# Performance work log

Hardware: AMD Instinct MI355X
Metric: run time of the kernel (lower is better)

The kernel has to match this reference:

```python
import jax, jax.numpy as jnp
import numpy as np

DIM = 64
HEADS = 4
DIM_HEAD = 32
HIDDEN = HEADS * DIM_HEAD  # 128
EPS = 1e-5


def _layernorm_ch(x, g, b):
    # channel-dim LayerNorm (biased var), x: [b, c, n]
    mean = jnp.mean(x, axis=1, keepdims=True)
    var = jnp.var(x, axis=1, keepdims=True)  # unbiased=False
    return (x - mean) / jnp.sqrt(var + EPS) * g.reshape(1, -1, 1) + b.reshape(1, -1, 1)


def setup_inputs() -> dict:
    key = jax.random.key(0)
    ks = jax.random.split(key, 4)
    x = jax.random.normal(ks[0], (2, DIM, 32, 64, 64), dtype=jnp.float32)
    # 1x1x1 convs are channel matmuls; store weights as [out_ch, in_ch]
    w_qkv = jax.random.normal(ks[1], (HIDDEN * 3, DIM), dtype=jnp.float32) * (1.0 / np.sqrt(DIM))
    w_out = jax.random.normal(ks[2], (DIM, HIDDEN), dtype=jnp.float32) * (1.0 / np.sqrt(HIDDEN))
    b_out = jax.random.normal(ks[3], (DIM,), dtype=jnp.float32) * 0.02
    g1 = jnp.ones((DIM,), dtype=jnp.float32)
    b1 = jnp.zeros((DIM,), dtype=jnp.float32)
    g2 = jnp.ones((DIM,), dtype=jnp.float32)
    b2 = jnp.zeros((DIM,), dtype=jnp.float32)
    return {"x": x, "g1": g1, "b1": b1, "w_qkv": w_qkv, "w_out": w_out,
            "b_out": b_out, "g2": g2, "b2": b2}


def reference(x, g1, b1, w_qkv, w_out, b_out, g2, b2):
    b, c, *spatial = x.shape
    n = int(np.prod(spatial))
    scale = DIM_HEAD ** -0.5

    xf = x.reshape(b, c, n)
    xn = _layernorm_ch(xf, g1, b1)

    # 1x1x1 conv qkv projection (no bias)
    qkv = jnp.einsum('oc,bcn->bon', w_qkv, xn)  # [b, 3*hidden, n]
    qkv = qkv.reshape(b, 3, HEADS, DIM_HEAD, n)
    q, k, v = qkv[:, 0], qkv[:, 1], qkv[:, 2]   # each [b, h, d, n]

    q = jax.nn.softmax(q, axis=2) * scale       # softmax over dim_head
    k = jax.nn.softmax(k, axis=3)               # softmax over tokens

    ctx = jnp.einsum('bhdn,bhen->bhde', k, v)   # [b, h, d, e] small
    out = jnp.einsum('bhde,bhdn->bhen', ctx, q) # [b, h, e, n]
    out = out.reshape(b, HIDDEN, n)

    y = jnp.einsum('oc,bcn->bon', w_out, out) + b_out.reshape(1, -1, 1)
    y = _layernorm_ch(y, g2, b2)
    return y.reshape(b, c, *spatial)
```

## Files before the change

### kernel.cpp

```cpp
#include <hip/hip_runtime.h>

#define NCOL 131072
#define CH 64

typedef float floatx4 __attribute__((ext_vector_type(4)));
typedef __bf16 bf16x8 __attribute__((ext_vector_type(8)));
typedef unsigned int u32x4 __attribute__((ext_vector_type(4)));
typedef unsigned int u32x2 __attribute__((ext_vector_type(2)));

union FragU { u32x4 q; bf16x8 v; unsigned short us[8]; };

__device__ __forceinline__ unsigned short bfb(float f){
  union { __bf16 h; unsigned short s; } u; u.h = (__bf16)f; return u.s;
}
__device__ __forceinline__ float bf2f(unsigned short h){
  union { unsigned u; float f; } x{(unsigned)h << 16};
  return x.f;
}

__device__ __forceinline__ void ln_stage(const float* __restrict__ xp,
    const float* __restrict__ g, const float* __restrict__ bb,
    unsigned short* __restrict__ xn_s, int t)
{
  float xv[64]; float s = 0.f, ss = 0.f;
  #pragma unroll
  for (int c = 0; c < 64; c++){ float u = xp[(long)c*NCOL]; xv[c] = u; s += u; ss = fmaf(u,u,ss); }
  const float mean = s * (1.f/64.f);
  const float rstd = rsqrtf(ss * (1.f/64.f) - mean*mean + 1e-5f);
  #pragma unroll
  for (int c = 0; c < 64; c++) xv[c] = (xv[c]-mean)*rstd*g[c] + bb[c];
  #pragma unroll
  for (int j = 0; j < 8; j++){
    FragU u;
    #pragma unroll
    for (int e = 0; e < 8; e++) u.v[e] = (__bf16)xv[j*8+e];
    *(u32x4*)(xn_s + t*72 + j*8) = u.q;
  }
}

__global__ __launch_bounds__(256) void kW(
    const float* __restrict__ wqkv, unsigned short* __restrict__ wbf, float* __restrict__ Oz)
{
  const int i = blockIdx.x*256 + threadIdx.x;
  wbf[i] = bfb(wqkv[i]);
  if (i < 8448) Oz[i] = 0.f;
}

__global__ __launch_bounds__(256) void kA(
    const float* __restrict__ x, const float* __restrict__ g1, const float* __restrict__ b1,
    const unsigned short* __restrict__ wbf, float* __restrict__ pctx, float* __restrict__ Zg)
{
  __shared__ __align__(16) char smem[37888];
  unsigned short* xn_s = (unsigned short*)smem;
  unsigned short* ek_s = (unsigned short*)smem;
  unsigned short* v_s  = (unsigned short*)(smem + 16896);
  float* Zp            = (float*)(smem + 33792);

  const int t = threadIdx.x;
  const int bid = blockIdx.x;
  const int b = bid >> 9;
  const long col0 = (long)(bid & 511) * 256;
  const int w = t >> 6, lane = t & 63, qq = lane >> 4, l16 = lane & 15;

  ln_stage(x + (long)b*CH*NCOL + col0 + t, g1, b1, xn_s, t);
  FragU bx[4][2];
  #pragma unroll
  for (int nt = 0; nt < 4; nt++)
    #pragma unroll
    for (int ks = 0; ks < 2; ks++)
      bx[nt][ks].q = *(const u32x4*)(xn_s + ((4*w+nt)*16 + l16)*72 + ks*32 + qq*8);
  __syncthreads();

  floatx4 cc[4][2][2];
  #pragma unroll
  for (int h = 0; h < 4; h++)
    #pragma unroll
    for (int dt = 0; dt < 2; dt++)
      #pragma unroll
      for (int et = 0; et < 2; et++)
        cc[h][dt][et] = floatx4{0.f,0.f,0.f,0.f};

  #pragma unroll
  for (int h = 0; h < 4; h++){
    float zr[8];
    #pragma unroll
    for (int j = 0; j < 8; j++) zr[j] = 0.f;
    #pragma unroll
    for (int rt = 0; rt < 4; rt++){
      const int row0 = ((rt < 2) ? 128 : 256) + h*32 + (rt & 1)*16;
      const unsigned short* wr = wbf + (row0 + l16)*64 + qq*8;
      FragU a0, a1;
      a0.q = *(const u32x4*)wr;
      a1.q = *(const u32x4*)(wr + 32);
      unsigned short* dst = ((rt < 2) ? ek_s : v_s) + ((rt & 1)*16 + qq*4)*264;
      #pragma unroll
      for (int nt = 0; nt < 4; nt++){
        floatx4 c = floatx4{0.f,0.f,0.f,0.f};
        c = __builtin_amdgcn_mfma_f32_16x16x32_bf16(a0.v, bx[nt][0].v, c, 0, 0, 0);
        c = __builtin_amdgcn_mfma_f32_16x16x32_bf16(a1.v, bx[nt][1].v, c, 0, 0, 0);
        const int colb = (4*w+nt)*16 + l16;
        if (rt < 2){
          #pragma unroll
          for (int r = 0; r < 4; r++){
            const float e = __expf(c[r]);
            dst[r*264 + colb] = bfb(e);
            zr[(rt & 1)*4 + r] += e;
          }
        } else {
          #pragma unroll
          for (int r = 0; r < 4; r++) dst[r*264 + colb] = bfb(c[r]);
        }
      }
    }
    #pragma unroll
    for (int j = 0; j < 8; j++){
      float v = zr[j];
      v += __shfl_xor(v, 1, 64); v += __shfl_xor(v, 2, 64);
      v += __shfl_xor(v, 4, 64); v += __shfl_xor(v, 8, 64);
      if (l16 == 0) Zp[w*128 + h*32 + (j >> 2)*16 + qq*4 + (j & 3)] = v;
    }
    #pragma unroll
    for (int kk = 0; kk < 2; kk++){
      const int ks2 = 2*w + kk;
      FragU ae[2], bv[2];
      #pragma unroll
      for (int dt = 0; dt < 2; dt++) ae[dt].q = *(const u32x4*)(ek_s + (dt*16 + l16)*264 + ks2*32 + qq*8);
      #pragma unroll
      for (int et = 0; et < 2; et++) bv[et].q = *(const u32x4*)(v_s + (et*16 + l16)*264 + ks2*32 + qq*8);
      #pragma unroll
      for (int dt = 0; dt < 2; dt++)
        #pragma unroll
        for (int et = 0; et < 2; et++)
          cc[h][dt][et] = __builtin_amdgcn_mfma_f32_16x16x32_bf16(ae[dt].v, bv[et].v, cc[h][dt][et], 0, 0, 0);
    }
  }
  __syncthreads();

  if (t < 128){
    const float z = Zp[t] + Zp[128 + t] + Zp[256 + t] + Zp[384 + t];
    atomicAdd(&Zg[b*128 + t], z);
  }

  float* scr = (float*)smem;
  if (w & 1){
    #pragma unroll
    for (int h = 0; h < 4; h++)
      #pragma unroll
      for (int dt = 0; dt < 2; dt++)
        #pragma unroll
        for (int et = 0; et < 2; et++)
          ((floatx4*)scr)[(w>>1)*1024 + (h*4 + dt*2 + et)*64 + lane] = cc[h][dt][et];
  }
  __syncthreads();
  if (!(w & 1)){
    #pragma unroll
    for (int h = 0; h < 4; h++)
      #pragma unroll
      for (int dt = 0; dt < 2; dt++)
        #pragma unroll
        for (int et = 0; et < 2; et++)
          cc[h][dt][et] += ((floatx4*)scr)[(w>>1)*1024 + (h*4 + dt*2 + et)*64 + lane];
  }
  __syncthreads();
  if (w == 2){
    #pragma unroll
    for (int h = 0; h < 4; h++)
      #pragma unroll
      for (int dt = 0; dt < 2; dt++)
        #pragma unroll
        for (int et = 0; et < 2; et++)
          ((floatx4*)scr)[(h*4 + dt*2 + et)*64 + lane] = cc[h][dt][et];
  }
  __syncthreads();
  if (w == 0){
    #pragma unroll
    for (int h = 0; h < 4; h++)
      #pragma unroll
      for (int dt = 0; dt < 2; dt++)
        #pragma unroll
        for (int et = 0; et < 2; et++){
          floatx4 r = cc[h][dt][et] + ((floatx4*)scr)[(h*4 + dt*2 + et)*64 + lane];
          *(floatx4*)(pctx + (long)bid*4096 + (h*4 + dt*2 + et)*256 + lane*4) = r;
        }
  }
}

__global__ __launch_bounds__(256) void kR1(
    const float* __restrict__ pctx, float* __restrict__ O)
{
  const int blk = blockIdx.x;
  const int b = blk >> 7;
  const int part = (blk >> 4) & 7;
  const int chunk = blk & 15;
  const int t = threadIdx.x;
  const int r = chunk*256 + t;
  const float* p = pctx + ((long)(b*512 + part*64))*4096 + r;
  float s = 0.f;
  #pragma unroll 16
  for (int row = 0; row < 64; row++) s += p[(long)row*4096];
  atomicAdd(&O[b*4096 + r], s);
}

__global__ __launch_bounds__(256) void kM(
    const float* __restrict__ O, const float* __restrict__ Zg,
    const float* __restrict__ wout, unsigned short* __restrict__ Mgbf)
{
  const int idx = blockIdx.x*256 + threadIdx.x;
  const int b = idx >> 13, rem = idx & 8191;
  const int h = rem >> 11, o = (rem >> 5) & 63, dd = rem & 31;
  const int dt = dd >> 4, qq = (dd >> 2) & 3, rg = dd & 3;
  float m = 0.f;
  #pragma unroll
  for (int ee = 0; ee < 32; ee++){
    const int et = ee >> 4, l16 = ee & 15;
    const int r = h*1024 + (dt*2 + et)*256 + (qq*16 + l16)*4 + rg;
    m = fmaf(wout[o*128 + h*32 + ee], O[b*4096 + r], m);
  }
  m /= Zg[b*128 + h*32 + dd];
  Mgbf[idx] = bfb(m);
}

__global__ __launch_bounds__(256) void kB(
    const float* __restrict__ x, const float* __restrict__ g1, const float* __restrict__ b1,
    const unsigned short* __restrict__ wbf, const unsigned short* __restrict__ Mgbf,
    const float* __restrict__ bout, const float* __restrict__ g2, const float* __restrict__ b2,
    float* __restrict__ y)
{
  __shared__ __align__(16) char smem[37632];
  unsigned short* xn_s = (unsigned short*)smem;
  unsigned short* qs_s = (unsigned short*)smem;
  float* sp            = (float*)(smem + 36864);

  const int t = threadIdx.x;
  const int bid = blockIdx.x;
  const int b = bid >> 9;
  const long col0 = (long)(bid & 511) * 256;
  const int w = t >> 6, lane = t & 63, qq = lane >> 4, l16 = lane & 15;

  if (t < 64){ sp[t] = bout[t]; sp[64+t] = g2[t]; sp[128+t] = b2[t]; }
  ln_stage(x + (long)b*CH*NCOL + col0 + t, g1, b1, xn_s, t);
  FragU bx[4][2];
  #pragma unroll
  for (int nt = 0; nt < 4; nt++)
    #pragma unroll
    for (int ks = 0; ks < 2; ks++)
      bx[nt][ks].q = *(const u32x4*)(xn_s + ((4*w+nt)*16 + l16)*72 + ks*32 + qq*8);
  __syncthreads();

  floatx4 yacc[4][4];
  #pragma unroll
  for (int ot = 0; ot < 4; ot++)
    #pragma unroll
    for (int nt = 0; nt < 4; nt++)
      yacc[ot][nt] = floatx4{0.f,0.f,0.f,0.f};

  #pragma unroll
  for (int h = 0; h < 4; h++){
    FragU a00, a01, a10, a11;
    {
      const unsigned short* wr0 = wbf + (h*32 + l16)*64 + qq*8;
      const unsigned short* wr1 = wbf + (h*32 + 16 + l16)*64 + qq*8;
      a00.q = *(const u32x4*)wr0; a01.q = *(const u32x4*)(wr0 + 32);
      a10.q = *(const u32x4*)wr1; a11.q = *(const u32x4*)(wr1 + 32);
    }
    #pragma unroll
    for (int nt = 0; nt < 4; nt++){
      floatx4 c0 = floatx4{0.f,0.f,0.f,0.f};
      floatx4 c1 = floatx4{0.f,0.f,0.f,0.f};
      c0 = __builtin_amdgcn_mfma_f32_16x16x32_bf16(a00.v, bx[nt][0].v, c0, 0, 0, 0);
      c0 = __builtin_amdgcn_mfma_f32_16x16x32_bf16(a01.v, bx[nt][1].v, c0, 0, 0, 0);
      c1 = __builtin_amdgcn_mfma_f32_16x16x32_bf16(a10.v, bx[nt][0].v, c1, 0, 0, 0);
      c1 = __builtin_amdgcn_mfma_f32_16x16x32_bf16(a11.v, bx[nt][1].v, c1, 0, 0, 0);
      float e[8]; float s = 0.f;
      #pragma unroll
      for (int r = 0; r < 4; r++){ e[r] = __expf(c0[r]); s += e[r]; }
      #pragma unroll
      for (int r = 0; r < 4; r++){ e[4+r] = __expf(c1[r]); s += e[4+r]; }
      s += __shfl_xor(s, 16, 64); s += __shfl_xor(s, 32, 64);
      const float sc = 0.17677669529663687f / s;
      const int colb = (4*w+nt)*16 + l16;
      u32x2 pk0, pk1;
      pk0[0] = (unsigned)bfb(e[0]*sc) | ((unsigned)bfb(e[1]*sc) << 16);
      pk0[1] = (unsigned)bfb(e[2]*sc) | ((unsigned)bfb(e[3]*sc) << 16);
      pk1[0] = (unsigned)bfb(e[4]*sc) | ((unsigned)bfb(e[5]*sc) << 16);
      pk1[1] = (unsigned)bfb(e[6]*sc) | ((unsigned)bfb(e[7]*sc) << 16);
      *(u32x2*)(qs_s + colb*40 + qq*4)      = pk0;
      *(u32x2*)(qs_s + colb*40 + 16 + qq*4) = pk1;
    }
    #pragma unroll
    for (int ot = 0; ot < 4; ot++){
      FragU am;
      am.q = *(const u32x4*)(Mgbf + (((long)b*4 + h)*64 + ot*16 + l16)*32 + qq*8);
      #pragma unroll
      for (int nt = 0; nt < 4; nt++){
        FragU bq; bq.q = *(const u32x4*)(qs_s + ((4*w+nt)*16 + l16)*40 + qq*8);
        yacc[ot][nt] = __builtin_amdgcn_mfma_f32_16x16x32_bf16(am.v, bq.v, yacc[ot][nt], 0, 0, 0);
      }
    }
  }

  const long ybase = (long)b*CH*NCOL;
  #pragma unroll
  for (int nt = 0; nt < 4; nt++){
    const long colg = col0 + (4*w+nt)*16 + l16;
    float vals[16]; float s = 0.f, ss = 0.f;
    #pragma unroll
    for (int ot = 0; ot < 4; ot++)
      #pragma unroll
      for (int r = 0; r < 4; r++){
        const float v = yacc[ot][nt][r] + sp[ot*16 + qq*4 + r];
        vals[ot*4+r] = v; s += v; ss = fmaf(v, v, ss);
      }
    s  += __shfl_xor(s, 16, 64);  s  += __shfl_xor(s, 32, 64);
    ss += __shfl_xor(ss, 16, 64); ss += __shfl_xor(ss, 32, 64);
    const float mean = s * (1.f/64.f);
    const float rstd = rsqrtf(ss * (1.f/64.f) - mean*mean + 1e-5f);
    #pragma unroll
    for (int ot = 0; ot < 4; ot++)
      #pragma unroll
      for (int r = 0; r < 4; r++){
        const int row = ot*16 + qq*4 + r;
        y[ybase + (long)row*NCOL + colg] = (vals[ot*4+r]-mean)*rstd*sp[64+row] + sp[128+row];
      }
  }
}

extern "C" void kernel_launch(void* const* d_in, const int* in_sizes, int n_in,
                              void* d_out, int out_size, void* d_ws, size_t ws_size,
                              hipStream_t stream)
{
  const float* x    = (const float*)d_in[0];
  const float* g1   = (const float*)d_in[1];
  const float* b1   = (const float*)d_in[2];
  const float* wqkv = (const float*)d_in[3];
  const float* wout = (const float*)d_in[4];
  const float* bout = (const float*)d_in[5];
  const float* g2   = (const float*)d_in[6];
  const float* b2   = (const float*)d_in[7];
  float* y  = (float*)d_out;
  float* ws = (float*)d_ws;

  float* pctx = ws;
  float* O    = ws + 4194304;
  float* Zg   = O + 8192;
  unsigned short* Mgbf = (unsigned short*)(Zg + 256);
  unsigned short* wbf  = (unsigned short*)(ws + 4210944);

  hipLaunchKernelGGL(kW,  dim3(96),   dim3(256), 0, stream, wqkv, wbf, O);
  hipLaunchKernelGGL(kA,  dim3(1024), dim3(256), 0, stream, x, g1, b1, wbf, pctx, Zg);
  hipLaunchKernelGGL(kR1, dim3(256),  dim3(256), 0, stream, pctx, O);
  hipLaunchKernelGGL(kM,  dim3(64),   dim3(256), 0, stream, O, Zg, wout, Mgbf);
  hipLaunchKernelGGL(kB,  dim3(1024), dim3(256), 0, stream, x, g1, b1, wbf, Mgbf, bout, g2, b2, y);
}
```

Baseline: 229.7 us.

## Replace partial-context buffer and reduction kernels with striped atomics and in-block M computation

kA now atomically adds its per-block context partials into 8 striped copies of the accumulator instead of writing a 16 MB partial buffer, so the kR1 reduction kernel is removed. The kM kernel is also folded into kB: every block sums the 8 stripes into shared memory, multiplies by w_out, divides by Zg, and keeps the bf16 M matrix in shared memory. This cuts two launches and a large global write/read, at the cost of atomic contention and redundant M computation in all 1024 kB blocks. Launch bounds for kA and kB also gain an occupancy hint of 4.

```diff
diff --git a/kernel.cpp b/kernel.cpp
--- a/kernel.cpp
+++ b/kernel.cpp
@@ -42,13 +42,13 @@
     const float* __restrict__ wqkv, unsigned short* __restrict__ wbf, float* __restrict__ Oz)
 {
   const int i = blockIdx.x*256 + threadIdx.x;
-  wbf[i] = bfb(wqkv[i]);
-  if (i < 8448) Oz[i] = 0.f;
-}
-
-__global__ __launch_bounds__(256) void kA(
+  if (i < 24576) wbf[i] = bfb(wqkv[i]);
+  if (i < 65792) Oz[i] = 0.f;
+}
+
+__global__ __launch_bounds__(256, 4) void kA(
     const float* __restrict__ x, const float* __restrict__ g1, const float* __restrict__ b1,
-    const unsigned short* __restrict__ wbf, float* __restrict__ pctx, float* __restrict__ Zg)
+    const unsigned short* __restrict__ wbf, float* __restrict__ O8, float* __restrict__ Zg)
 {
   __shared__ __align__(16) char smem[37888];
   unsigned short* xn_s = (unsigned short*)smem;
@@ -173,6 +173,7 @@
   }
   __syncthreads();
   if (w == 0){
+    const long obase = ((long)b*8 + (bid & 7))*4096;
     #pragma unroll
     for (int h = 0; h < 4; h++)
       #pragma unroll
@@ -180,55 +181,25 @@
         #pragma unroll
         for (int et = 0; et < 2; et++){
           floatx4 r = cc[h][dt][et] + ((floatx4*)scr)[(h*4 + dt*2 + et)*64 + lane];
-          *(floatx4*)(pctx + (long)bid*4096 + (h*4 + dt*2 + et)*256 + lane*4) = r;
+          const long p = obase + (h*4 + dt*2 + et)*256 + lane*4;
+          #pragma unroll
+          for (int j = 0; j < 4; j++) atomicAdd(&O8[p + j], r[j]);
         }
   }
 }
 
-__global__ __launch_bounds__(256) void kR1(
-    const float* __restrict__ pctx, float* __restrict__ O)
-{
-  const int blk = blockIdx.x;
-  const int b = blk >> 7;
-  const int part = (blk >> 4) & 7;
-  const int chunk = blk & 15;
-  const int t = threadIdx.x;
-  const int r = chunk*256 + t;
-  const float* p = pctx + ((long)(b*512 + part*64))*4096 + r;
-  float s = 0.f;
-  #pragma unroll 16
-  for (int row = 0; row < 64; row++) s += p[(long)row*4096];
-  atomicAdd(&O[b*4096 + r], s);
-}
-
-__global__ __launch_bounds__(256) void kM(
-    const float* __restrict__ O, const float* __restrict__ Zg,
-    const float* __restrict__ wout, unsigned short* __restrict__ Mgbf)
-{
-  const int idx = blockIdx.x*256 + threadIdx.x;
-  const int b = idx >> 13, rem = idx & 8191;
-  const int h = rem >> 11, o = (rem >> 5) & 63, dd = rem & 31;
-  const int dt = dd >> 4, qq = (dd >> 2) & 3, rg = dd & 3;
-  float m = 0.f;
-  #pragma unroll
-  for (int ee = 0; ee < 32; ee++){
-    const int et = ee >> 4, l16 = ee & 15;
-    const int r = h*1024 + (dt*2 + et)*256 + (qq*16 + l16)*4 + rg;
-    m = fmaf(wout[o*128 + h*32 + ee], O[b*4096 + r], m);
-  }
-  m /= Zg[b*128 + h*32 + dd];
-  Mgbf[idx] = bfb(m);
-}
-
-__global__ __launch_bounds__(256) void kB(
+__global__ __launch_bounds__(256, 4) void kB(
     const float* __restrict__ x, const float* __restrict__ g1, const float* __restrict__ b1,
-    const unsigned short* __restrict__ wbf, const unsigned short* __restrict__ Mgbf,
+    const unsigned short* __restrict__ wbf, const float* __restrict__ O8,
+    const float* __restrict__ Zg, const float* __restrict__ wout,
     const float* __restrict__ bout, const float* __restrict__ g2, const float* __restrict__ b2,
     float* __restrict__ y)
 {
   __shared__ __align__(16) char smem[37632];
   unsigned short* xn_s = (unsigned short*)smem;
+  float* O_s           = (float*)smem;
   unsigned short* qs_s = (unsigned short*)smem;
+  unsigned short* Mg_s = (unsigned short*)(smem + 20480);
   float* sp            = (float*)(smem + 36864);
 
   const int t = threadIdx.x;
@@ -245,6 +216,43 @@
     #pragma unroll
     for (int ks = 0; ks < 2; ks++)
       bx[nt][ks].q = *(const u32x4*)(xn_s + ((4*w+nt)*16 + l16)*72 + ks*32 + qq*8);
+  __syncthreads();
+
+  {
+    const float* Ob = O8 + (long)b*8*4096;
+    #pragma unroll
+    for (int j = 0; j < 4; j++){
+      floatx4 a = floatx4{0.f,0.f,0.f,0.f};
+      #pragma unroll
+      for (int s8 = 0; s8 < 8; s8++)
+        a += ((const floatx4*)(Ob + s8*4096))[j*256 + t];
+      ((floatx4*)O_s)[j*256 + t] = a;
+    }
+    __syncthreads();
+
+    const int h = t >> 6, o = t & 63;
+    float wrow[32];
+    #pragma unroll
+    for (int ee = 0; ee < 32; ee++) wrow[ee] = wout[o*128 + h*32 + ee];
+    #pragma unroll
+    for (int j2 = 0; j2 < 16; j2++){
+      float m01[2];
+      #pragma unroll
+      for (int half = 0; half < 2; half++){
+        const int dd = j2*2 + half;
+        const int dt = dd >> 4, qq2 = (dd >> 2) & 3, rg2 = dd & 3;
+        float m = 0.f;
+        #pragma unroll
+        for (int ee = 0; ee < 32; ee++){
+          const int et = ee >> 4, l16e = ee & 15;
+          m = fmaf(wrow[ee], O_s[h*1024 + (dt*2+et)*256 + (qq2*16+l16e)*4 + rg2], m);
+        }
+        m01[half] = m / Zg[b*128 + h*32 + dd];
+      }
+      *(unsigned*)(Mg_s + (h*64 + o)*32 + j2*2) =
+          (unsigned)bfb(m01[0]) | ((unsigned)bfb(m01[1]) << 16);
+    }
+  }
   __syncthreads();
 
   floatx4 yacc[4][4];
@@ -290,7 +298,7 @@
     #pragma unroll
     for (int ot = 0; ot < 4; ot++){
       FragU am;
-      am.q = *(const u32x4*)(Mgbf + (((long)b*4 + h)*64 + ot*16 + l16)*32 + qq*8);
+      am.q = *(const u32x4*)(Mg_s + (h*64 + ot*16 + l16)*32 + qq*8);
       #pragma unroll
       for (int nt = 0; nt < 4; nt++){
         FragU bq; bq.q = *(const u32x4*)(qs_s + ((4*w+nt)*16 + l16)*40 + qq*8);
@@ -340,15 +348,11 @@
   float* y  = (float*)d_out;
   float* ws = (float*)d_ws;
 
-  float* pctx = ws;
-  float* O    = ws + 4194304;
-  float* Zg   = O + 8192;
-  unsigned short* Mgbf = (unsigned short*)(Zg + 256);
-  unsigned short* wbf  = (unsigned short*)(ws + 4210944);
-
-  hipLaunchKernelGGL(kW,  dim3(96),   dim3(256), 0, stream, wqkv, wbf, O);
-  hipLaunchKernelGGL(kA,  dim3(1024), dim3(256), 0, stream, x, g1, b1, wbf, pctx, Zg);
-  hipLaunchKernelGGL(kR1, dim3(256),  dim3(256), 0, stream, pctx, O);
-  hipLaunchKernelGGL(kM,  dim3(64),   dim3(256), 0, stream, O, Zg, wout, Mgbf);
-  hipLaunchKernelGGL(kB,  dim3(1024), dim3(256), 0, stream, x, g1, b1, wbf, Mgbf, bout, g2, b2, y);
-}
+  float* O8 = ws;
+  float* Zg = ws + 65536;
+  unsigned short* wbf = (unsigned short*)(ws + 65792);
+
+  hipLaunchKernelGGL(kW, dim3(384),  dim3(256), 0, stream, wqkv, wbf, O8);
+  hipLaunchKernelGGL(kA, dim3(1024), dim3(256), 0, stream, x, g1, b1, wbf, O8, Zg);
+  hipLaunchKernelGGL(kB, dim3(1024), dim3(256), 0, stream, x, g1, b1, wbf, O8, Zg, wout, bout, g2, b2, y);
+}
```

After: 301.5 us. 1.31x slower.

## Materialize softmaxed q in global memory during kA, drop recompute in final kernel

Applied to the files above, without the earlier changes.

The first pass now computes the q projection and its softmax and stores the scaled q to global memory as bf16. The final kernel reads that q and a shared-memory copy of the folded output matrix, skipping the second LayerNorm and q projection over x. This trades recompute for an extra write and read of a tensor about the size of x, adding global memory traffic to a likely bandwidth-bound pipeline.

```diff
diff --git a/kernel.cpp b/kernel.cpp
--- a/kernel.cpp
+++ b/kernel.cpp
@@ -48,7 +48,8 @@
 
 __global__ __launch_bounds__(256) void kA(
     const float* __restrict__ x, const float* __restrict__ g1, const float* __restrict__ b1,
-    const unsigned short* __restrict__ wbf, float* __restrict__ pctx, float* __restrict__ Zg)
+    const unsigned short* __restrict__ wbf, float* __restrict__ pctx, float* __restrict__ Zg,
+    unsigned short* __restrict__ qsg)
 {
   __shared__ __align__(16) char smem[37888];
   unsigned short* xn_s = (unsigned short*)smem;
@@ -70,6 +71,42 @@
     for (int ks = 0; ks < 2; ks++)
       bx[nt][ks].q = *(const u32x4*)(xn_s + ((4*w+nt)*16 + l16)*72 + ks*32 + qq*8);
   __syncthreads();
+
+  #pragma unroll
+  for (int h = 0; h < 4; h++){
+    FragU a00, a01, a10, a11;
+    {
+      const unsigned short* wr0 = wbf + (h*32 + l16)*64 + qq*8;
+      const unsigned short* wr1 = wbf + (h*32 + 16 + l16)*64 + qq*8;
+      a00.q = *(const u32x4*)wr0; a01.q = *(const u32x4*)(wr0 + 32);
+      a10.q = *(const u32x4*)wr1; a11.q = *(const u32x4*)(wr1 + 32);
+    }
+    #pragma unroll
+    for (int nt = 0; nt < 4; nt++){
+      floatx4 c0 = floatx4{0.f,0.f,0.f,0.f};
+      floatx4 c1 = floatx4{0.f,0.f,0.f,0.f};
+      c0 = __builtin_amdgcn_mfma_f32_16x16x32_bf16(a00.v, bx[nt][0].v, c0, 0, 0, 0);
+      c0 = __builtin_amdgcn_mfma_f32_16x16x32_bf16(a01.v, bx[nt][1].v, c0, 0, 0, 0);
+      c1 = __builtin_amdgcn_mfma_f32_16x16x32_bf16(a10.v, bx[nt][0].v, c1, 0, 0, 0);
+      c1 = __builtin_amdgcn_mfma_f32_16x16x32_bf16(a11.v, bx[nt][1].v, c1, 0, 0, 0);
+      float e[8]; float s = 0.f;
+      #pragma unroll
+      for (int r = 0; r < 4; r++){ e[r] = __expf(c0[r]); s += e[r]; }
+      #pragma unroll
+      for (int r = 0; r < 4; r++){ e[4+r] = __expf(c1[r]); s += e[4+r]; }
+      s += __shfl_xor(s, 16, 64); s += __shfl_xor(s, 32, 64);
+      const float sc = 0.17677669529663687f / s;
+      const int colb = (4*w+nt)*16 + l16;
+      unsigned short* qg = qsg + (((long)b*NCOL + col0 + colb)*32 + (long)h*NCOL*64);
+      u32x2 pk0, pk1;
+      pk0[0] = (unsigned)bfb(e[0]*sc) | ((unsigned)bfb(e[1]*sc) << 16);
+      pk0[1] = (unsigned)bfb(e[2]*sc) | ((unsigned)bfb(e[3]*sc) << 16);
+      pk1[0] = (unsigned)bfb(e[4]*sc) | ((unsigned)bfb(e[5]*sc) << 16);
+      pk1[1] = (unsigned)bfb(e[6]*sc) | ((unsigned)bfb(e[7]*sc) << 16);
+      *(u32x2*)(qg + qq*4)      = pk0;
+      *(u32x2*)(qg + 16 + qq*4) = pk1;
+    }
+  }
 
   floatx4 cc[4][2][2];
   #pragma unroll
@@ -220,16 +257,14 @@
   Mgbf[idx] = bfb(m);
 }
 
-__global__ __launch_bounds__(256) void kB(
-    const float* __restrict__ x, const float* __restrict__ g1, const float* __restrict__ b1,
-    const unsigned short* __restrict__ wbf, const unsigned short* __restrict__ Mgbf,
+__global__ __launch_bounds__(256) void kC(
+    const unsigned short* __restrict__ qsg, const unsigned short* __restrict__ Mgbf,
     const float* __restrict__ bout, const float* __restrict__ g2, const float* __restrict__ b2,
     float* __restrict__ y)
 {
-  __shared__ __align__(16) char smem[37632];
-  unsigned short* xn_s = (unsigned short*)smem;
-  unsigned short* qs_s = (unsigned short*)smem;
-  float* sp            = (float*)(smem + 36864);
+  __shared__ __align__(16) char smem[17152];
+  unsigned short* Mg_s = (unsigned short*)smem;
+  float* sp            = (float*)(smem + 16384);
 
   const int t = threadIdx.x;
   const int bid = blockIdx.x;
@@ -238,13 +273,9 @@
   const int w = t >> 6, lane = t & 63, qq = lane >> 4, l16 = lane & 15;
 
   if (t < 64){ sp[t] = bout[t]; sp[64+t] = g2[t]; sp[128+t] = b2[t]; }
-  ln_stage(x + (long)b*CH*NCOL + col0 + t, g1, b1, xn_s, t);
-  FragU bx[4][2];
-  #pragma unroll
-  for (int nt = 0; nt < 4; nt++)
-    #pragma unroll
-    for (int ks = 0; ks < 2; ks++)
-      bx[nt][ks].q = *(const u32x4*)(xn_s + ((4*w+nt)*16 + l16)*72 + ks*32 + qq*8);
+  #pragma unroll
+  for (int j = 0; j < 4; j++)
+    ((u32x4*)Mg_s)[j*256 + t] = ((const u32x4*)(Mgbf + (long)b*8192))[j*256 + t];
   __syncthreads();
 
   floatx4 yacc[4][4];
@@ -256,46 +287,18 @@
 
   #pragma unroll
   for (int h = 0; h < 4; h++){
-    FragU a00, a01, a10, a11;
-    {
-      const unsigned short* wr0 = wbf + (h*32 + l16)*64 + qq*8;
-      const unsigned short* wr1 = wbf + (h*32 + 16 + l16)*64 + qq*8;
-      a00.q = *(const u32x4*)wr0; a01.q = *(const u32x4*)(wr0 + 32);
-      a10.q = *(const u32x4*)wr1; a11.q = *(const u32x4*)(wr1 + 32);
-    }
-    #pragma unroll
-    for (int nt = 0; nt < 4; nt++){
-      floatx4 c0 = floatx4{0.f,0.f,0.f,0.f};
-      floatx4 c1 = floatx4{0.f,0.f,0.f,0.f};
-      c0 = __builtin_amdgcn_mfma_f32_16x16x32_bf16(a00.v, bx[nt][0].v, c0, 0, 0, 0);
-      c0 = __builtin_amdgcn_mfma_f32_16x16x32_bf16(a01.v, bx[nt][1].v, c0, 0, 0, 0);
-      c1 = __builtin_amdgcn_mfma_f32_16x16x32_bf16(a10.v, bx[nt][0].v, c1, 0, 0, 0);
-      c1 = __builtin_amdgcn_mfma_f32_16x16x32_bf16(a11.v, bx[nt][1].v, c1, 0, 0, 0);
-      float e[8]; float s = 0.f;
-      #pragma unroll
-      for (int r = 0; r < 4; r++){ e[r] = __expf(c0[r]); s += e[r]; }
-      #pragma unroll
-      for (int r = 0; r < 4; r++){ e[4+r] = __expf(c1[r]); s += e[4+r]; }
-      s += __shfl_xor(s, 16, 64); s += __shfl_xor(s, 32, 64);
-      const float sc = 0.17677669529663687f / s;
-      const int colb = (4*w+nt)*16 + l16;
-      u32x2 pk0, pk1;
-      pk0[0] = (unsigned)bfb(e[0]*sc) | ((unsigned)bfb(e[1]*sc) << 16);
-      pk0[1] = (unsigned)bfb(e[2]*sc) | ((unsigned)bfb(e[3]*sc) << 16);
-      pk1[0] = (unsigned)bfb(e[4]*sc) | ((unsigned)bfb(e[5]*sc) << 16);
-      pk1[1] = (unsigned)bfb(e[6]*sc) | ((unsigned)bfb(e[7]*sc) << 16);
-      *(u32x2*)(qs_s + colb*40 + qq*4)      = pk0;
-      *(u32x2*)(qs_s + colb*40 + 16 + qq*4) = pk1;
-    }
+    FragU bq[4];
+    #pragma unroll
+    for (int nt = 0; nt < 4; nt++)
+      bq[nt].q = *(const u32x4*)(qsg + ((long)b*NCOL + col0 + (4*w+nt)*16 + l16)*32
+                                      + (long)h*NCOL*64 + qq*8);
     #pragma unroll
     for (int ot = 0; ot < 4; ot++){
       FragU am;
-      am.q = *(const u32x4*)(Mgbf + (((long)b*4 + h)*64 + ot*16 + l16)*32 + qq*8);
-      #pragma unroll
-      for (int nt = 0; nt < 4; nt++){
-        FragU bq; bq.q = *(const u32x4*)(qs_s + ((4*w+nt)*16 + l16)*40 + qq*8);
-        yacc[ot][nt] = __builtin_amdgcn_mfma_f32_16x16x32_bf16(am.v, bq.v, yacc[ot][nt], 0, 0, 0);
-      }
+      am.q = *(const u32x4*)(Mg_s + (h*64 + ot*16 + l16)*32 + qq*8);
+      #pragma unroll
+      for (int nt = 0; nt < 4; nt++)
+        yacc[ot][nt] = __builtin_amdgcn_mfma_f32_16x16x32_bf16(am.v, bq[nt].v, yacc[ot][nt], 0, 0, 0);
     }
   }
 
@@ -342,13 +345,14 @@
 
   float* pctx = ws;
   float* O    = ws + 4194304;
-  float* Zg   = O + 8192;
-  unsigned short* Mgbf = (unsigned short*)(Zg + 256);
-  unsigned short* wbf  = (unsigned short*)(ws + 4210944);
+  float* Zg   = ws + 4202496;
+  unsigned short* wbf  = (unsigned short*)(ws + 4202752);
+  unsigned short* Mgbf = (unsigned short*)(ws + 4215040);
+  unsigned short* qsg  = (unsigned short*)(ws + 4223232);
 
   hipLaunchKernelGGL(kW,  dim3(96),   dim3(256), 0, stream, wqkv, wbf, O);
-  hipLaunchKernelGGL(kA,  dim3(1024), dim3(256), 0, stream, x, g1, b1, wbf, pctx, Zg);
+  hipLaunchKernelGGL(kA,  dim3(1024), dim3(256), 0, stream, x, g1, b1, wbf, pctx, Zg, qsg);
   hipLaunchKernelGGL(kR1, dim3(256),  dim3(256), 0, stream, pctx, O);
   hipLaunchKernelGGL(kM,  dim3(64),   dim3(256), 0, stream, O, Zg, wout, Mgbf);
-  hipLaunchKernelGGL(kB,  dim3(1024), dim3(256), 0, stream, x, g1, b1, wbf, Mgbf, bout, g2, b2, y);
-}
+  hipLaunchKernelGGL(kC,  dim3(1024), dim3(256), 0, stream, qsg, Mgbf, bout, g2, b2, y);
+}
```

After: 216.2 us. 5.9% less time.
